# Kernel tuning notes

Measured on AMD Instinct MI355X. Metric: run time of the kernel, lower is better.

The kernel has to match this reference:

```python
import jax, jax.numpy as jnp
import numpy as np

N = 100000      # nodes
E = 1_600_000   # edges (avg degree 16)
IN, HID, OUT = 64, 64, 32


def setup_inputs() -> dict:
    key = jax.random.key(0)
    k1, k2, k3, k4, k5, k6 = jax.random.split(key, 6)
    x = jax.random.uniform(k1, (N, IN), dtype=jnp.float32)
    edge_index = jax.random.randint(k2, (2, E), 0, N, dtype=jnp.int32)
    # GCNConv weights (glorot-ish scale) and biases
    W1 = jax.random.normal(k3, (IN, HID), dtype=jnp.float32) * (1.0 / np.sqrt(IN))
    b1 = jnp.zeros((HID,), dtype=jnp.float32)
    W2 = jax.random.normal(k4, (HID, OUT), dtype=jnp.float32) * (1.0 / np.sqrt(HID))
    b2 = jnp.zeros((OUT,), dtype=jnp.float32)
    return {"x": x, "edge_index": edge_index, "W1": W1, "b1": b1, "W2": W2, "b2": b2}


def reference(x, edge_index, W1, b1, W2, b2):
    n = x.shape[0]
    # PyG GCNConv: add self-loops, symmetric deg^{-1/2} normalization
    loops = jnp.arange(n, dtype=edge_index.dtype)
    src = jnp.concatenate([edge_index[0], loops])  # message sources
    dst = jnp.concatenate([edge_index[1], loops])  # message targets
    ones = jnp.ones(src.shape[0], dtype=x.dtype)
    deg = jax.ops.segment_sum(ones, dst, num_segments=n)
    dinv = jnp.where(deg > 0, jax.lax.rsqrt(deg), 0.0)
    norm = dinv[src] * dinv[dst]  # [E+N]

    def gcn_conv(h, W, b):
        h = h @ W                          # [n, d_out]
        msg = h[src] * norm[:, None]       # gather + edge-normalize
        agg = jax.ops.segment_sum(msg, dst, num_segments=n)  # scatter-add
        return agg + b

    h = jax.nn.relu(gcn_conv(x, W1, b1))
    return gcn_conv(h, W2, b2)
```

## Files before the change

### kernel.cpp

```cpp
#include <hip/hip_runtime.h>
#include <hip/hip_fp16.h>


#define BSHIFT 8
#define BNODES 256
#define NB 256
#define CAP 5120

union H8 {
    uint4 u;
    __half2 h[4];
};

__global__ __launch_bounds__(256) void scatter_kernel(
    const int* __restrict__ src, const int* __restrict__ dst,
    int* __restrict__ cur, int* __restrict__ buf, int E) {
    __shared__ int h[512];
    __shared__ int curl[512];
    int t = threadIdx.x, b = blockIdx.x;
    for (int i = t; i < 512; i += 256) h[i] = 0;
    __syncthreads();
    int per = (E + NB - 1) / NB;
    int lo = b * per;
    int hi = min(lo + per, E);
    for (int i = lo + t; i < hi; i += 256) atomicAdd(&h[dst[i] >> BSHIFT], 1);
    __syncthreads();
    for (int i = t; i < 512; i += 256) {
        int c = h[i];
        curl[i] = c ? atomicAdd(&cur[i], c) : 0;
    }
    __syncthreads();
    for (int i = lo + t; i < hi; i += 256) {
        int d = dst[i];
        int bin = d >> BSHIFT;
        int loc = atomicAdd(&curl[bin], 1);
        if (loc < CAP)
            buf[(size_t)bin * CAP + loc] = (src[i] << BSHIFT) | (d & (BNODES - 1));
    }
}

__global__ __launch_bounds__(256) void bsortgemm1_kernel(
    const int* __restrict__ cur, int* __restrict__ buf,
    int2* __restrict__ off2, float* __restrict__ dinv,
    const float* __restrict__ x, const float* __restrict__ W1,
    __half* __restrict__ hsh, int N) {
    __shared__ int stage[CAP];
    __shared__ int h[BNODES];
    __shared__ int c2[BNODES];
    __shared__ float4 Ws[64 * 16];
    int t = threadIdx.x, b = blockIdx.x;
    int cnt = min(cur[b], CAP);
    int base = b * CAP;
    for (int i = t; i < cnt; i += 256) stage[i] = buf[base + i];
    h[t] = 0;
    __syncthreads();
    for (int i = t; i < cnt; i += 256)
        atomicAdd(&h[stage[i] & (BNODES - 1)], 1);
    __syncthreads();
    int deg = h[t];
#pragma unroll
    for (int d = 1; d < BNODES; d <<= 1) {
        int v = (t >= d) ? h[t - d] : 0;
        __syncthreads();
        h[t] += v;
        __syncthreads();
    }
    int excl = h[t] - deg;
    c2[t] = excl;
    int node = (b << BSHIFT) + t;
    bool valid = node < N;
    float di = rsqrtf((float)(deg + 1));
    if (valid) {
        off2[node] = make_int2(base + excl, base + excl + deg);
        dinv[node] = di;
    }
    __syncthreads();
    for (int i = t; i < cnt; i += 256) {
        int p = stage[i];
        int pos = atomicAdd(&c2[p & (BNODES - 1)], 1);
        buf[base + pos] = p >> BSHIFT;
    }
    const float4* W4 = (const float4*)W1;
    for (int i = t; i < 1024; i += 256) Ws[i] = W4[i];
    __syncthreads();
    if (!valid) return;
    const float4* xr = (const float4*)(x + (size_t)node * 64);
    float4 acc[16];
#pragma unroll
    for (int j = 0; j < 16; j++) acc[j] = make_float4(0.f, 0.f, 0.f, 0.f);
    for (int k4 = 0; k4 < 16; k4++) {
        float4 xv = xr[k4];
#pragma unroll
        for (int kk = 0; kk < 4; kk++) {
            float a = ((const float*)&xv)[kk];
            const float4* wr = &Ws[(k4 * 4 + kk) * 16];
#pragma unroll
            for (int j = 0; j < 16; j++) {
                float4 w = wr[j];
                acc[j].x += a * w.x; acc[j].y += a * w.y;
                acc[j].z += a * w.z; acc[j].w += a * w.w;
            }
        }
    }
    uint4* ha = (uint4*)(hsh + (size_t)node * 64);
#pragma unroll
    for (int j = 0; j < 8; j++) {
        H8 p;
        float4 v0 = acc[2 * j], v1 = acc[2 * j + 1];
        p.h[0] = __floats2half2_rn(v0.x * di, v0.y * di);
        p.h[1] = __floats2half2_rn(v0.z * di, v0.w * di);
        p.h[2] = __floats2half2_rn(v1.x * di, v1.y * di);
        p.h[3] = __floats2half2_rn(v1.z * di, v1.w * di);
        ha[j] = p.u;
    }
}

__global__ __launch_bounds__(256) void agg1gemm2_kernel(
    const uint4* __restrict__ hsh4, const int* __restrict__ ssrc,
    const int2* __restrict__ off2, const float* __restrict__ dinv,
    const float* __restrict__ b1, const float* __restrict__ W2,
    __half* __restrict__ gsh, int N) {
    __shared__ uint4 h1s[32][9];
    __shared__ float4 Ws2[64 * 8];
    int t = threadIdx.x;
    const float4* W24 = (const float4*)W2;
    for (int i = t; i < 512; i += 256) Ws2[i] = W24[i];
    int lane = t & 63;
    int wid = (blockIdx.x * 256 + t) >> 6;
    int node = wid * 8 + (lane >> 3);
    int fi = lane & 7;
    int nl = t >> 3;
    if (node < N) {
        H8 sv;
        sv.u = hsh4[(size_t)node * 8 + fi];
        float2 a0 = __half22float2(sv.h[0]);
        float2 a1 = __half22float2(sv.h[1]);
        float2 a2 = __half22float2(sv.h[2]);
        float2 a3 = __half22float2(sv.h[3]);
        float2 c0 = make_float2(0.f, 0.f), c1 = make_float2(0.f, 0.f);
        float2 c2 = make_float2(0.f, 0.f), c3 = make_float2(0.f, 0.f);
        int2 lh = off2[node];
        int lo = lh.x, hi = lh.y;
        int e = lo;
        for (; e + 8 <= hi; e += 8) {
            int s0 = __builtin_nontemporal_load(&ssrc[e + 0]);
            int s1 = __builtin_nontemporal_load(&ssrc[e + 1]);
            int s2 = __builtin_nontemporal_load(&ssrc[e + 2]);
            int s3 = __builtin_nontemporal_load(&ssrc[e + 3]);
            int s4 = __builtin_nontemporal_load(&ssrc[e + 4]);
            int s5 = __builtin_nontemporal_load(&ssrc[e + 5]);
            int s6 = __builtin_nontemporal_load(&ssrc[e + 6]);
            int s7 = __builtin_nontemporal_load(&ssrc[e + 7]);
            H8 v0, v1, v2, v3, v4, v5, v6, v7;
            v0.u = hsh4[(size_t)s0 * 8 + fi];
            v1.u = hsh4[(size_t)s1 * 8 + fi];
            v2.u = hsh4[(size_t)s2 * 8 + fi];
            v3.u = hsh4[(size_t)s3 * 8 + fi];
            v4.u = hsh4[(size_t)s4 * 8 + fi];
            v5.u = hsh4[(size_t)s5 * 8 + fi];
            v6.u = hsh4[(size_t)s6 * 8 + fi];
            v7.u = hsh4[(size_t)s7 * 8 + fi];
#pragma unroll
            for (int q = 0; q < 4; q++) {
                float2* aA = (q == 0) ? &a0 : (q == 1) ? &a1 : (q == 2) ? &a2 : &a3;
                float2* cA = (q == 0) ? &c0 : (q == 1) ? &c1 : (q == 2) ? &c2 : &c3;
                float2 f0 = __half22float2(v0.h[q]);
                float2 f1 = __half22float2(v1.h[q]);
                float2 f2 = __half22float2(v2.h[q]);
                float2 f3 = __half22float2(v3.h[q]);
                float2 f4 = __half22float2(v4.h[q]);
                float2 f5 = __half22float2(v5.h[q]);
                float2 f6 = __half22float2(v6.h[q]);
                float2 f7 = __half22float2(v7.h[q]);
                aA->x += (f0.x + f1.x) + (f2.x + f3.x);
                aA->y += (f0.y + f1.y) + (f2.y + f3.y);
                cA->x += (f4.x + f5.x) + (f6.x + f7.x);
                cA->y += (f4.y + f5.y) + (f6.y + f7.y);
            }
        }
        for (; e < hi; e++) {
            H8 v;
            v.u = hsh4[(size_t)__builtin_nontemporal_load(&ssrc[e]) * 8 + fi];
            float2 f0 = __half22float2(v.h[0]);
            float2 f1 = __half22float2(v.h[1]);
            float2 f2 = __half22float2(v.h[2]);
            float2 f3 = __half22float2(v.h[3]);
            c0.x += f0.x; c0.y += f0.y;
            c1.x += f1.x; c1.y += f1.y;
            c2.x += f2.x; c2.y += f2.y;
            c3.x += f3.x; c3.y += f3.y;
        }
        float di = dinv[node];
        float4 bl = ((const float4*)b1)[fi * 2];
        float4 bh = ((const float4*)b1)[fi * 2 + 1];
        float r0 = fmaxf((a0.x + c0.x) * di + bl.x, 0.f);
        float r1 = fmaxf((a0.y + c0.y) * di + bl.y, 0.f);
        float r2 = fmaxf((a1.x + c1.x) * di + bl.z, 0.f);
        float r3 = fmaxf((a1.y + c1.y) * di + bl.w, 0.f);
        float r4 = fmaxf((a2.x + c2.x) * di + bh.x, 0.f);
        float r5 = fmaxf((a2.y + c2.y) * di + bh.y, 0.f);
        float r6 = fmaxf((a3.x + c3.x) * di + bh.z, 0.f);
        float r7 = fmaxf((a3.y + c3.y) * di + bh.w, 0.f);
        H8 p;
        p.h[0] = __floats2half2_rn(r0, r1);
        p.h[1] = __floats2half2_rn(r2, r3);
        p.h[2] = __floats2half2_rn(r4, r5);
        p.h[3] = __floats2half2_rn(r6, r7);
        h1s[nl][fi] = p.u;
    }
    __syncthreads();
    int gn = blockIdx.x * 32 + nl;
    if (gn < N) {
        const __half2* hr = (const __half2*)&h1s[nl][0];
        int o = t & 7;
        float4 acc = make_float4(0.f, 0.f, 0.f, 0.f);
#pragma unroll
        for (int k2 = 0; k2 < 32; k2++) {
            float2 f = __half22float2(hr[k2]);
            float4 w0 = Ws2[(2 * k2) * 8 + o];
            float4 w1 = Ws2[(2 * k2 + 1) * 8 + o];
            acc.x += f.x * w0.x + f.y * w1.x;
            acc.y += f.x * w0.y + f.y * w1.y;
            acc.z += f.x * w0.z + f.y * w1.z;
            acc.w += f.x * w0.w + f.y * w1.w;
        }
        float dg = dinv[gn];
        union { uint2 u; __half2 h[2]; } pk;
        pk.h[0] = __floats2half2_rn(acc.x * dg, acc.y * dg);
        pk.h[1] = __floats2half2_rn(acc.z * dg, acc.w * dg);
        ((uint2*)(gsh + (size_t)gn * 32))[o] = pk.u;
    }
}

__global__ __launch_bounds__(256) void agg2_kernel(
    const uint4* __restrict__ gsh4, const int* __restrict__ ssrc,
    const int2* __restrict__ off2, const float* __restrict__ dinv,
    const float* __restrict__ b2, float4* __restrict__ out4, int N) {
    int lane = threadIdx.x & 63;
    int wid = (blockIdx.x * 256 + threadIdx.x) >> 6;
    int node = wid * 16 + (lane >> 2);
    int fi = lane & 3;
    if (node >= N) return;
    H8 sv;
    sv.u = gsh4[(size_t)node * 4 + fi];
    float2 a0 = __half22float2(sv.h[0]);
    float2 a1 = __half22float2(sv.h[1]);
    float2 a2 = __half22float2(sv.h[2]);
    float2 a3 = __half22float2(sv.h[3]);
    float2 c0 = make_float2(0.f, 0.f), c1 = make_float2(0.f, 0.f);
    float2 c2 = make_float2(0.f, 0.f), c3 = make_float2(0.f, 0.f);
    int2 lh = off2[node];
    int lo = lh.x, hi = lh.y;
    int e = lo;
    for (; e + 8 <= hi; e += 8) {
        int s0 = __builtin_nontemporal_load(&ssrc[e + 0]);
        int s1 = __builtin_nontemporal_load(&ssrc[e + 1]);
        int s2 = __builtin_nontemporal_load(&ssrc[e + 2]);
        int s3 = __builtin_nontemporal_load(&ssrc[e + 3]);
        int s4 = __builtin_nontemporal_load(&ssrc[e + 4]);
        int s5 = __builtin_nontemporal_load(&ssrc[e + 5]);
        int s6 = __builtin_nontemporal_load(&ssrc[e + 6]);
        int s7 = __builtin_nontemporal_load(&ssrc[e + 7]);
        H8 v0, v1, v2, v3, v4, v5, v6, v7;
        v0.u = gsh4[(size_t)s0 * 4 + fi];
        v1.u = gsh4[(size_t)s1 * 4 + fi];
        v2.u = gsh4[(size_t)s2 * 4 + fi];
        v3.u = gsh4[(size_t)s3 * 4 + fi];
        v4.u = gsh4[(size_t)s4 * 4 + fi];
        v5.u = gsh4[(size_t)s5 * 4 + fi];
        v6.u = gsh4[(size_t)s6 * 4 + fi];
        v7.u = gsh4[(size_t)s7 * 4 + fi];
#pragma unroll
        for (int q = 0; q < 4; q++) {
            float2* aA = (q == 0) ? &a0 : (q == 1) ? &a1 : (q == 2) ? &a2 : &a3;
            float2* cA = (q == 0) ? &c0 : (q == 1) ? &c1 : (q == 2) ? &c2 : &c3;
            float2 f0 = __half22float2(v0.h[q]);
            float2 f1 = __half22float2(v1.h[q]);
            float2 f2 = __half22float2(v2.h[q]);
            float2 f3 = __half22float2(v3.h[q]);
            float2 f4 = __half22float2(v4.h[q]);
            float2 f5 = __half22float2(v5.h[q]);
            float2 f6 = __half22float2(v6.h[q]);
            float2 f7 = __half22float2(v7.h[q]);
            aA->x += (f0.x + f1.x) + (f2.x + f3.x);
            aA->y += (f0.y + f1.y) + (f2.y + f3.y);
            cA->x += (f4.x + f5.x) + (f6.x + f7.x);
            cA->y += (f4.y + f5.y) + (f6.y + f7.y);
        }
    }
    for (; e < hi; e++) {
        H8 v;
        v.u = gsh4[(size_t)__builtin_nontemporal_load(&ssrc[e]) * 4 + fi];
        float2 f0 = __half22float2(v.h[0]);
        float2 f1 = __half22float2(v.h[1]);
        float2 f2 = __half22float2(v.h[2]);
        float2 f3 = __half22float2(v.h[3]);
        c0.x += f0.x; c0.y += f0.y;
        c1.x += f1.x; c1.y += f1.y;
        c2.x += f2.x; c2.y += f2.y;
        c3.x += f3.x; c3.y += f3.y;
    }
    float di = dinv[node];
    float4 bl = ((const float4*)b2)[fi * 2];
    float4 bh = ((const float4*)b2)[fi * 2 + 1];
    float4 r0, r1;
    r0.x = (a0.x + c0.x) * di + bl.x;
    r0.y = (a0.y + c0.y) * di + bl.y;
    r0.z = (a1.x + c1.x) * di + bl.z;
    r0.w = (a1.y + c1.y) * di + bl.w;
    r1.x = (a2.x + c2.x) * di + bh.x;
    r1.y = (a2.y + c2.y) * di + bh.y;
    r1.z = (a3.x + c3.x) * di + bh.z;
    r1.w = (a3.y + c3.y) * di + bh.w;
    out4[(size_t)node * 8 + fi * 2 + 0] = r0;
    out4[(size_t)node * 8 + fi * 2 + 1] = r1;
}

extern "C" void kernel_launch(void* const* d_in, const int* in_sizes, int n_in,
                              void* d_out, int out_size, void* d_ws,
                              size_t ws_size, hipStream_t stream) {
    const float* x  = (const float*)d_in[0];
    const int* ei   = (const int*)d_in[1];
    const float* W1 = (const float*)d_in[2];
    const float* b1 = (const float*)d_in[3];
    const float* W2 = (const float*)d_in[4];
    const float* b2 = (const float*)d_in[5];
    int N = in_sizes[0] / 64;
    int E = in_sizes[1] / 2;
    const int* src = ei;
    const int* dst = ei + E;
    int B = (N + BNODES - 1) >> BSHIFT;

    char* ws = (char*)d_ws;
    size_t o = 0;
    auto align16 = [&o]() { o = (o + 15) & ~(size_t)15; };
    int* cur    = (int*)(ws + o); o += 512 * 4; align16();
    int* buf    = (int*)(ws + o); o += (size_t)B * CAP * 4; align16();
    int2* off2  = (int2*)(ws + o); o += (size_t)N * 8; align16();
    float* dinv = (float*)(ws + o); o += (size_t)N * 4; align16();
    __half* hsh = (__half*)(ws + o); o += (size_t)N * 64 * 2; align16();
    __half* gsh = (__half*)(ws + o); o += (size_t)N * 32 * 2; align16();
    float* outp = (float*)d_out;

    hipMemsetAsync(cur, 0, 512 * 4, stream);
    scatter_kernel<<<NB, 256, 0, stream>>>(src, dst, cur, buf, E);
    bsortgemm1_kernel<<<B, 256, 0, stream>>>(cur, buf, off2, dinv, x, W1, hsh,
                                             N);
    agg1gemm2_kernel<<<(N + 31) / 32, 256, 0, stream>>>(
        (const uint4*)hsh, buf, off2, dinv, b1, W2, gsh, N);
    agg2_kernel<<<(N + 63) / 64, 256, 0, stream>>>(
        (const uint4*)gsh, buf, off2, dinv, b2, (float4*)outp, N);
}
```

Before: 219.1 us.

## Use masked 8-wide gather loops and shuffle-based layer-2 GEMM without LDS staging

Replaces the unrolled-by-8 gather loop plus scalar remainder loop in both aggregation kernels with one 8-wide loop. Out-of-range edges in the last chunk are clamped to the last index and multiplied by a 0/1 mask, so the whole node's neighbours go through the wide path. In the fused agg1+GEMM2 kernel, the LDS staging buffer and its barrier are dropped. Each 8-lane group exchanges the layer-1 activations with width-8 shuffles and computes the 64x32 projection per lane. This trades extra redundant loads and multiplies on tail chunks for better memory-level parallelism and less synchronisation.

```diff
diff --git a/kernel.cpp b/kernel.cpp
--- a/kernel.cpp
+++ b/kernel.cpp
@@ -11,6 +11,17 @@
     uint4 u;
     __half2 h[4];
 };
+
+__device__ inline float2 u2f2(unsigned u) {
+    union { unsigned x; __half2 h; } c;
+    c.x = u;
+    return __half22float2(c.h);
+}
+__device__ inline unsigned f2u(float a, float b) {
+    union { unsigned x; __half2 h; } c;
+    c.h = __floats2half2_rn(a, b);
+    return c.x;
+}
 
 __global__ __launch_bounds__(256) void scatter_kernel(
     const int* __restrict__ src, const int* __restrict__ dst,
@@ -120,156 +131,57 @@
     const int2* __restrict__ off2, const float* __restrict__ dinv,
     const float* __restrict__ b1, const float* __restrict__ W2,
     __half* __restrict__ gsh, int N) {
-    __shared__ uint4 h1s[32][9];
     __shared__ float4 Ws2[64 * 8];
     int t = threadIdx.x;
     const float4* W24 = (const float4*)W2;
     for (int i = t; i < 512; i += 256) Ws2[i] = W24[i];
+    __syncthreads();
     int lane = t & 63;
     int wid = (blockIdx.x * 256 + t) >> 6;
     int node = wid * 8 + (lane >> 3);
     int fi = lane & 7;
-    int nl = t >> 3;
-    if (node < N) {
-        H8 sv;
-        sv.u = hsh4[(size_t)node * 8 + fi];
-        float2 a0 = __half22float2(sv.h[0]);
-        float2 a1 = __half22float2(sv.h[1]);
-        float2 a2 = __half22float2(sv.h[2]);
-        float2 a3 = __half22float2(sv.h[3]);
-        float2 c0 = make_float2(0.f, 0.f), c1 = make_float2(0.f, 0.f);
-        float2 c2 = make_float2(0.f, 0.f), c3 = make_float2(0.f, 0.f);
-        int2 lh = off2[node];
-        int lo = lh.x, hi = lh.y;
-        int e = lo;
-        for (; e + 8 <= hi; e += 8) {
-            int s0 = __builtin_nontemporal_load(&ssrc[e + 0]);
-            int s1 = __builtin_nontemporal_load(&ssrc[e + 1]);
-            int s2 = __builtin_nontemporal_load(&ssrc[e + 2]);
-            int s3 = __builtin_nontemporal_load(&ssrc[e + 3]);
-            int s4 = __builtin_nontemporal_load(&ssrc[e + 4]);
-            int s5 = __builtin_nontemporal_load(&ssrc[e + 5]);
-            int s6 = __builtin_nontemporal_load(&ssrc[e + 6]);
-            int s7 = __builtin_nontemporal_load(&ssrc[e + 7]);
-            H8 v0, v1, v2, v3, v4, v5, v6, v7;
-            v0.u = hsh4[(size_t)s0 * 8 + fi];
-            v1.u = hsh4[(size_t)s1 * 8 + fi];
-            v2.u = hsh4[(size_t)s2 * 8 + fi];
-            v3.u = hsh4[(size_t)s3 * 8 + fi];
-            v4.u = hsh4[(size_t)s4 * 8 + fi];
-            v5.u = hsh4[(size_t)s5 * 8 + fi];
-            v6.u = hsh4[(size_t)s6 * 8 + fi];
-            v7.u = hsh4[(size_t)s7 * 8 + fi];
-#pragma unroll
-            for (int q = 0; q < 4; q++) {
-                float2* aA = (q == 0) ? &a0 : (q == 1) ? &a1 : (q == 2) ? &a2 : &a3;
-                float2* cA = (q == 0) ? &c0 : (q == 1) ? &c1 : (q == 2) ? &c2 : &c3;
-                float2 f0 = __half22float2(v0.h[q]);
-                float2 f1 = __half22float2(v1.h[q]);
-                float2 f2 = __half22float2(v2.h[q]);
-                float2 f3 = __half22float2(v3.h[q]);
-                float2 f4 = __half22float2(v4.h[q]);
-                float2 f5 = __half22float2(v5.h[q]);
-                float2 f6 = __half22float2(v6.h[q]);
-                float2 f7 = __half22float2(v7.h[q]);
-                aA->x += (f0.x + f1.x) + (f2.x + f3.x);
-                aA->y += (f0.y + f1.y) + (f2.y + f3.y);
-                cA->x += (f4.x + f5.x) + (f6.x + f7.x);
-                cA->y += (f4.y + f5.y) + (f6.y + f7.y);
-            }
-        }
-        for (; e < hi; e++) {
-            H8 v;
-            v.u = hsh4[(size_t)__builtin_nontemporal_load(&ssrc[e]) * 8 + fi];
-            float2 f0 = __half22float2(v.h[0]);
-            float2 f1 = __half22float2(v.h[1]);
-            float2 f2 = __half22float2(v.h[2]);
-            float2 f3 = __half22float2(v.h[3]);
-            c0.x += f0.x; c0.y += f0.y;
-            c1.x += f1.x; c1.y += f1.y;
-            c2.x += f2.x; c2.y += f2.y;
-            c3.x += f3.x; c3.y += f3.y;
-        }
-        float di = dinv[node];
-        float4 bl = ((const float4*)b1)[fi * 2];
-        float4 bh = ((const float4*)b1)[fi * 2 + 1];
-        float r0 = fmaxf((a0.x + c0.x) * di + bl.x, 0.f);
-        float r1 = fmaxf((a0.y + c0.y) * di + bl.y, 0.f);
-        float r2 = fmaxf((a1.x + c1.x) * di + bl.z, 0.f);
-        float r3 = fmaxf((a1.y + c1.y) * di + bl.w, 0.f);
-        float r4 = fmaxf((a2.x + c2.x) * di + bh.x, 0.f);
-        float r5 = fmaxf((a2.y + c2.y) * di + bh.y, 0.f);
-        float r6 = fmaxf((a3.x + c3.x) * di + bh.z, 0.f);
-        float r7 = fmaxf((a3.y + c3.y) * di + bh.w, 0.f);
-        H8 p;
-        p.h[0] = __floats2half2_rn(r0, r1);
-        p.h[1] = __floats2half2_rn(r2, r3);
-        p.h[2] = __floats2half2_rn(r4, r5);
-        p.h[3] = __floats2half2_rn(r6, r7);
-        h1s[nl][fi] = p.u;
-    }
-    __syncthreads();
-    int gn = blockIdx.x * 32 + nl;
-    if (gn < N) {
-        const __half2* hr = (const __half2*)&h1s[nl][0];
-        int o = t & 7;
-        float4 acc = make_float4(0.f, 0.f, 0.f, 0.f);
-#pragma unroll
-        for (int k2 = 0; k2 < 32; k2++) {
-            float2 f = __half22float2(hr[k2]);
-            float4 w0 = Ws2[(2 * k2) * 8 + o];
-            float4 w1 = Ws2[(2 * k2 + 1) * 8 + o];
-            acc.x += f.x * w0.x + f.y * w1.x;
-            acc.y += f.x * w0.y + f.y * w1.y;
-            acc.z += f.x * w0.z + f.y * w1.z;
-            acc.w += f.x * w0.w + f.y * w1.w;
-        }
-        float dg = dinv[gn];
-        union { uint2 u; __half2 h[2]; } pk;
-        pk.h[0] = __floats2half2_rn(acc.x * dg, acc.y * dg);
-        pk.h[1] = __floats2half2_rn(acc.z * dg, acc.w * dg);
-        ((uint2*)(gsh + (size_t)gn * 32))[o] = pk.u;
-    }
-}
-
-__global__ __launch_bounds__(256) void agg2_kernel(
-    const uint4* __restrict__ gsh4, const int* __restrict__ ssrc,
-    const int2* __restrict__ off2, const float* __restrict__ dinv,
-    const float* __restrict__ b2, float4* __restrict__ out4, int N) {
-    int lane = threadIdx.x & 63;
-    int wid = (blockIdx.x * 256 + threadIdx.x) >> 6;
-    int node = wid * 16 + (lane >> 2);
-    int fi = lane & 3;
     if (node >= N) return;
+    int2 lh = off2[node];
+    int lo = lh.x, hi = lh.y;
+    float di = dinv[node];
     H8 sv;
-    sv.u = gsh4[(size_t)node * 4 + fi];
+    sv.u = hsh4[(size_t)node * 8 + fi];
     float2 a0 = __half22float2(sv.h[0]);
     float2 a1 = __half22float2(sv.h[1]);
     float2 a2 = __half22float2(sv.h[2]);
     float2 a3 = __half22float2(sv.h[3]);
     float2 c0 = make_float2(0.f, 0.f), c1 = make_float2(0.f, 0.f);
     float2 c2 = make_float2(0.f, 0.f), c3 = make_float2(0.f, 0.f);
-    int2 lh = off2[node];
-    int lo = lh.x, hi = lh.y;
-    int e = lo;
-    for (; e + 8 <= hi; e += 8) {
-        int s0 = __builtin_nontemporal_load(&ssrc[e + 0]);
-        int s1 = __builtin_nontemporal_load(&ssrc[e + 1]);
-        int s2 = __builtin_nontemporal_load(&ssrc[e + 2]);
-        int s3 = __builtin_nontemporal_load(&ssrc[e + 3]);
-        int s4 = __builtin_nontemporal_load(&ssrc[e + 4]);
-        int s5 = __builtin_nontemporal_load(&ssrc[e + 5]);
-        int s6 = __builtin_nontemporal_load(&ssrc[e + 6]);
-        int s7 = __builtin_nontemporal_load(&ssrc[e + 7]);
+    int hm1 = hi - 1;
+    for (int e = lo; e < hi; e += 8) {
+        int i0 = e, i1 = min(e + 1, hm1), i2 = min(e + 2, hm1),
+            i3 = min(e + 3, hm1);
+        int i4 = min(e + 4, hm1), i5 = min(e + 5, hm1), i6 = min(e + 6, hm1),
+            i7 = min(e + 7, hm1);
+        int s0 = __builtin_nontemporal_load(&ssrc[i0]);
+        int s1 = __builtin_nontemporal_load(&ssrc[i1]);
+        int s2 = __builtin_nontemporal_load(&ssrc[i2]);
+        int s3 = __builtin_nontemporal_load(&ssrc[i3]);
+        int s4 = __builtin_nontemporal_load(&ssrc[i4]);
+        int s5 = __builtin_nontemporal_load(&ssrc[i5]);
+        int s6 = __builtin_nontemporal_load(&ssrc[i6]);
+        int s7 = __builtin_nontemporal_load(&ssrc[i7]);
         H8 v0, v1, v2, v3, v4, v5, v6, v7;
-        v0.u = gsh4[(size_t)s0 * 4 + fi];
-        v1.u = gsh4[(size_t)s1 * 4 + fi];
-        v2.u = gsh4[(size_t)s2 * 4 + fi];
-        v3.u = gsh4[(size_t)s3 * 4 + fi];
-        v4.u = gsh4[(size_t)s4 * 4 + fi];
-        v5.u = gsh4[(size_t)s5 * 4 + fi];
-        v6.u = gsh4[(size_t)s6 * 4 + fi];
-        v7.u = gsh4[(size_t)s7 * 4 + fi];
+        v0.u = hsh4[(size_t)s0 * 8 + fi];
+        v1.u = hsh4[(size_t)s1 * 8 + fi];
+        v2.u = hsh4[(size_t)s2 * 8 + fi];
+        v3.u = hsh4[(size_t)s3 * 8 + fi];
+        v4.u = hsh4[(size_t)s4 * 8 + fi];
+        v5.u = hsh4[(size_t)s5 * 8 + fi];
+        v6.u = hsh4[(size_t)s6 * 8 + fi];
+        v7.u = hsh4[(size_t)s7 * 8 + fi];
+        float m1 = (e + 1 < hi) ? 1.f : 0.f;
+        float m2 = (e + 2 < hi) ? 1.f : 0.f;
+        float m3 = (e + 3 < hi) ? 1.f : 0.f;
+        float m4 = (e + 4 < hi) ? 1.f : 0.f;
+        float m5 = (e + 5 < hi) ? 1.f : 0.f;
+        float m6 = (e + 6 < hi) ? 1.f : 0.f;
+        float m7 = (e + 7 < hi) ? 1.f : 0.f;
 #pragma unroll
         for (int q = 0; q < 4; q++) {
             float2* aA = (q == 0) ? &a0 : (q == 1) ? &a1 : (q == 2) ? &a2 : &a3;
@@ -282,25 +194,133 @@
             float2 f5 = __half22float2(v5.h[q]);
             float2 f6 = __half22float2(v6.h[q]);
             float2 f7 = __half22float2(v7.h[q]);
-            aA->x += (f0.x + f1.x) + (f2.x + f3.x);
-            aA->y += (f0.y + f1.y) + (f2.y + f3.y);
-            cA->x += (f4.x + f5.x) + (f6.x + f7.x);
-            cA->y += (f4.y + f5.y) + (f6.y + f7.y);
+            aA->x += f0.x + m1 * f1.x + m2 * f2.x + m3 * f3.x;
+            aA->y += f0.y + m1 * f1.y + m2 * f2.y + m3 * f3.y;
+            cA->x += m4 * f4.x + m5 * f5.x + m6 * f6.x + m7 * f7.x;
+            cA->y += m4 * f4.y + m5 * f5.y + m6 * f6.y + m7 * f7.y;
         }
     }
-    for (; e < hi; e++) {
-        H8 v;
-        v.u = gsh4[(size_t)__builtin_nontemporal_load(&ssrc[e]) * 4 + fi];
-        float2 f0 = __half22float2(v.h[0]);
-        float2 f1 = __half22float2(v.h[1]);
-        float2 f2 = __half22float2(v.h[2]);
-        float2 f3 = __half22float2(v.h[3]);
-        c0.x += f0.x; c0.y += f0.y;
-        c1.x += f1.x; c1.y += f1.y;
-        c2.x += f2.x; c2.y += f2.y;
-        c3.x += f3.x; c3.y += f3.y;
-    }
+    float4 bl = ((const float4*)b1)[fi * 2];
+    float4 bh = ((const float4*)b1)[fi * 2 + 1];
+    float r0 = fmaxf((a0.x + c0.x) * di + bl.x, 0.f);
+    float r1 = fmaxf((a0.y + c0.y) * di + bl.y, 0.f);
+    float r2 = fmaxf((a1.x + c1.x) * di + bl.z, 0.f);
+    float r3 = fmaxf((a1.y + c1.y) * di + bl.w, 0.f);
+    float r4 = fmaxf((a2.x + c2.x) * di + bh.x, 0.f);
+    float r5 = fmaxf((a2.y + c2.y) * di + bh.y, 0.f);
+    float r6 = fmaxf((a3.x + c3.x) * di + bh.z, 0.f);
+    float r7 = fmaxf((a3.y + c3.y) * di + bh.w, 0.f);
+    unsigned pk0 = f2u(r0, r1), pk1 = f2u(r2, r3);
+    unsigned pk2 = f2u(r4, r5), pk3 = f2u(r6, r7);
+    float4 acc2 = make_float4(0.f, 0.f, 0.f, 0.f);
+#pragma unroll
+    for (int s = 0; s < 8; s++) {
+        int sl = (fi + s) & 7;
+        unsigned u0 = __shfl(pk0, sl, 8);
+        unsigned u1 = __shfl(pk1, sl, 8);
+        unsigned u2 = __shfl(pk2, sl, 8);
+        unsigned u3 = __shfl(pk3, sl, 8);
+        float2 f0 = u2f2(u0), f1 = u2f2(u1), f2 = u2f2(u2), f3 = u2f2(u3);
+        const float4* wr = &Ws2[sl * 64 + fi];
+        float4 w;
+        w = wr[0];
+        acc2.x += f0.x * w.x; acc2.y += f0.x * w.y;
+        acc2.z += f0.x * w.z; acc2.w += f0.x * w.w;
+        w = wr[8];
+        acc2.x += f0.y * w.x; acc2.y += f0.y * w.y;
+        acc2.z += f0.y * w.z; acc2.w += f0.y * w.w;
+        w = wr[16];
+        acc2.x += f1.x * w.x; acc2.y += f1.x * w.y;
+        acc2.z += f1.x * w.z; acc2.w += f1.x * w.w;
+        w = wr[24];
+        acc2.x += f1.y * w.x; acc2.y += f1.y * w.y;
+        acc2.z += f1.y * w.z; acc2.w += f1.y * w.w;
+        w = wr[32];
+        acc2.x += f2.x * w.x; acc2.y += f2.x * w.y;
+        acc2.z += f2.x * w.z; acc2.w += f2.x * w.w;
+        w = wr[40];
+        acc2.x += f2.y * w.x; acc2.y += f2.y * w.y;
+        acc2.z += f2.y * w.z; acc2.w += f2.y * w.w;
+        w = wr[48];
+        acc2.x += f3.x * w.x; acc2.y += f3.x * w.y;
+        acc2.z += f3.x * w.z; acc2.w += f3.x * w.w;
+        w = wr[56];
+        acc2.x += f3.y * w.x; acc2.y += f3.y * w.y;
+        acc2.z += f3.y * w.z; acc2.w += f3.y * w.w;
+    }
+    uint2 pg;
+    pg.x = f2u(acc2.x * di, acc2.y * di);
+    pg.y = f2u(acc2.z * di, acc2.w * di);
+    ((uint2*)gsh)[(size_t)node * 8 + fi] = pg;
+}
+
+__global__ __launch_bounds__(256) void agg2_kernel(
+    const uint4* __restrict__ gsh4, const int* __restrict__ ssrc,
+    const int2* __restrict__ off2, const float* __restrict__ dinv,
+    const float* __restrict__ b2, float4* __restrict__ out4, int N) {
+    int lane = threadIdx.x & 63;
+    int wid = (blockIdx.x * 256 + threadIdx.x) >> 6;
+    int node = wid * 16 + (lane >> 2);
+    int fi = lane & 3;
+    if (node >= N) return;
+    int2 lh = off2[node];
+    int lo = lh.x, hi = lh.y;
     float di = dinv[node];
+    H8 sv;
+    sv.u = gsh4[(size_t)node * 4 + fi];
+    float2 a0 = __half22float2(sv.h[0]);
+    float2 a1 = __half22float2(sv.h[1]);
+    float2 a2 = __half22float2(sv.h[2]);
+    float2 a3 = __half22float2(sv.h[3]);
+    float2 c0 = make_float2(0.f, 0.f), c1 = make_float2(0.f, 0.f);
+    float2 c2 = make_float2(0.f, 0.f), c3 = make_float2(0.f, 0.f);
+    int hm1 = hi - 1;
+    for (int e = lo; e < hi; e += 8) {
+        int i1 = min(e + 1, hm1), i2 = min(e + 2, hm1), i3 = min(e + 3, hm1);
+        int i4 = min(e + 4, hm1), i5 = min(e + 5, hm1), i6 = min(e + 6, hm1),
+            i7 = min(e + 7, hm1);
+        int s0 = __builtin_nontemporal_load(&ssrc[e]);
+        int s1 = __builtin_nontemporal_load(&ssrc[i1]);
+        int s2 = __builtin_nontemporal_load(&ssrc[i2]);
+        int s3 = __builtin_nontemporal_load(&ssrc[i3]);
+        int s4 = __builtin_nontemporal_load(&ssrc[i4]);
+        int s5 = __builtin_nontemporal_load(&ssrc[i5]);
+        int s6 = __builtin_nontemporal_load(&ssrc[i6]);
+        int s7 = __builtin_nontemporal_load(&ssrc[i7]);
+        H8 v0, v1, v2, v3, v4, v5, v6, v7;
+        v0.u = gsh4[(size_t)s0 * 4 + fi];
+        v1.u = gsh4[(size_t)s1 * 4 + fi];
+        v2.u = gsh4[(size_t)s2 * 4 + fi];
+        v3.u = gsh4[(size_t)s3 * 4 + fi];
+        v4.u = gsh4[(size_t)s4 * 4 + fi];
+        v5.u = gsh4[(size_t)s5 * 4 + fi];
+        v6.u = gsh4[(size_t)s6 * 4 + fi];
+        v7.u = gsh4[(size_t)s7 * 4 + fi];
+        float m1 = (e + 1 < hi) ? 1.f : 0.f;
+        float m2 = (e + 2 < hi) ? 1.f : 0.f;
+        float m3 = (e + 3 < hi) ? 1.f : 0.f;
+        float m4 = (e + 4 < hi) ? 1.f : 0.f;
+        float m5 = (e + 5 < hi) ? 1.f : 0.f;
+        float m6 = (e + 6 < hi) ? 1.f : 0.f;
+        float m7 = (e + 7 < hi) ? 1.f : 0.f;
+#pragma unroll
+        for (int q = 0; q < 4; q++) {
+            float2* aA = (q == 0) ? &a0 : (q == 1) ? &a1 : (q == 2) ? &a2 : &a3;
+            float2* cA = (q == 0) ? &c0 : (q == 1) ? &c1 : (q == 2) ? &c2 : &c3;
+            float2 f0 = __half22float2(v0.h[q]);
+            float2 f1 = __half22float2(v1.h[q]);
+            float2 f2 = __half22float2(v2.h[q]);
+            float2 f3 = __half22float2(v3.h[q]);
+            float2 f4 = __half22float2(v4.h[q]);
+            float2 f5 = __half22float2(v5.h[q]);
+            float2 f6 = __half22float2(v6.h[q]);
+            float2 f7 = __half22float2(v7.h[q]);
+            aA->x += f0.x + m1 * f1.x + m2 * f2.x + m3 * f3.x;
+            aA->y += f0.y + m1 * f1.y + m2 * f2.y + m3 * f3.y;
+            cA->x += m4 * f4.x + m5 * f5.x + m6 * f6.x + m7 * f7.x;
+            cA->y += m4 * f4.y + m5 * f5.y + m6 * f6.y + m7 * f7.y;
+        }
+    }
     float4 bl = ((const float4*)b2)[fi * 2];
     float4 bh = ((const float4*)b2)[fi * 2 + 1];
     float4 r0, r1;
```

Measured after the change: 208.1 us. -5.0%, faster.
